# Kernel tuning notes

Hardware: AMD Instinct MI355X
Metric: run time of the kernel (lower is better)

The kernel has to match this reference:

```python
import jax, jax.numpy as jnp
import numpy as np

EPS = 1e-6
AREA_WIDTH = 3
NHEAD = 8
DIM = 16


def _skew(v):
    # v: [N,3] -> [N,3,3] cross-product matrix
    x, y, z = v[..., 0], v[..., 1], v[..., 2]
    zero = jnp.zeros_like(x)
    return jnp.stack([
        jnp.stack([zero, -z, y], -1),
        jnp.stack([z, zero, -x], -1),
        jnp.stack([-y, x, zero], -1)], -2)


def _create_meshgrid(h, w):
    # kornia create_meshgrid(..., normalized=False): last dim is (x, y), row-major flatten
    xs = jnp.arange(w, dtype=jnp.float32)
    ys = jnp.arange(h, dtype=jnp.float32)
    gx, gy = jnp.meshgrid(xs, ys, indexing='xy')  # [h,w]
    return jnp.stack([gx, gy], -1).reshape(h * w, 2)  # [S,2]


def _epipolar_lines(coord, R, t, K0, K1):
    # coord [S,2]; R [N,3,3]; t [N,3,1] -> lines [N,S,3] (unit-normalized a,b), mode [N,S]
    S = coord.shape[0]
    p = jnp.concatenate([coord, jnp.ones((S, 1), coord.dtype)], -1)  # [S,3]
    E = _skew(t[..., 0]) @ R                                         # [t]_x R
    F = jnp.swapaxes(jnp.linalg.inv(K1), -1, -2) @ E @ jnp.linalg.inv(K0)
    lines = jnp.einsum('nij,sj->nsi', F, p)
    n = jnp.linalg.norm(lines[..., :2], axis=-1, keepdims=True)
    lines = lines / jnp.maximum(n, 1e-12)
    mode = jnp.abs(lines[..., 1]) >= jnp.abs(lines[..., 0])  # True: solve y(x) (|b|>=|a|)
    return lines, mode


def _get_mask(lines, mode, coord, area_width):
    # lines [N,L,3], mode [N,L], coord [S,2] -> within [N,L,S]
    a, b, c = lines[..., 0], lines[..., 1], lines[..., 2]
    xs, ys = coord[:, 0], coord[:, 1]
    hw = area_width / 2.0
    safe = lambda d: jnp.where(jnp.abs(d) < 1e-12, 1e-12, d)
    cy = (-a / safe(b))[..., None] * xs + (-c / safe(b))[..., None]  # [N,L,S]
    cx = (-b / safe(a))[..., None] * ys + (-c / safe(a))[..., None]
    wy = (ys < cy + hw) & (ys > cy - hw)
    wx = (xs < cx + hw) & (xs > cx - hw)
    return jnp.where(mode[..., None], wy, wx)


def _gather_index(within, C):
    # sort-based top-C compaction, index 0 doubles as padding (faithful to source)
    S = within.shape[-1]
    idx = jnp.arange(S, dtype=jnp.int32)
    ti = jnp.where(within, idx[None, None, :], 0)
    ti = jnp.sort(ti, axis=-1)[..., -C:]
    return ti, ti != 0


def _feature_map(x):
    return jax.nn.elu(x) + 1.0


def reference(queries, keys, values, solved_sample, K0, K1, R, t, h0c, w0c, scale):
    N, L, H, D = queries.shape
    sol = np.asarray(solved_sample).astype(bool)  # static split of the batch
    sol_idx = np.nonzero(sol)[0]
    uns_idx = np.nonzero(~sol)[0]
    Q = _feature_map(queries)
    K = _feature_map(keys)
    out = jnp.zeros((N, L, H, D), queries.dtype)

    if sol_idx.size > 0:  # epipolar-gathered candidate attention, direction '0to1'
        coord = _create_meshgrid(h0c, w0c)
        K0s = K0[sol_idx].at[:, :2, :].mul(1.0 / scale)
        K1s = K1[sol_idx].at[:, :2, :].mul(1.0 / scale)
        C = max(h0c, w0c) * AREA_WIDTH
        lines, mode = _epipolar_lines(coord, R[sol_idx], t[sol_idx], K0s, K1s)
        within = _get_mask(lines, mode, coord, AREA_WIDTH)       # [Ns,L,S]
        index, mask = _gather_index(within, C)                    # [Ns,L,C]
        Ns = sol_idx.size
        n_ix = jnp.arange(Ns)[:, None, None]
        Qs = Q[sol_idx]
        Ks = K[sol_idx][n_ix, index]            # [Ns,L,C,H,D]
        Vs = values[sol_idx][n_ix, index]
        m = mask[..., None, None].astype(Ks.dtype)
        Ks = Ks * m
        Vs = Vs * m / C
        KV = jnp.einsum('nlchd,nlchv->nlhdv', Ks, Vs)
        Z = 1.0 / (jnp.einsum('nlhd,nlhd->nlh', Qs, Ks.sum(2)) + EPS)
        out = out.at[sol_idx].set(jnp.einsum('nlhd,nlhdv,nlh->nlhv', Qs, KV, Z) * C)

    if uns_idx.size > 0:  # plain linear attention
        Qu, Ku, Vu = Q[uns_idx], K[uns_idx], values[uns_idx]
        S = Ku.shape[1]
        KV = jnp.einsum('nshd,nshv->nhdv', Ku, Vu / S)
        Z = 1.0 / (jnp.einsum('nlhd,nhd->nlh', Qu, Ku.sum(1)) + EPS)
        out = out.at[uns_idx].set(jnp.einsum('nlhd,nhdv,nlh->nlhv', Qu, KV, Z) * S)
    return out


def setup_inputs() -> dict:
    key = jax.random.key(0)
    kq, kk, kv = jax.random.split(key, 3)
    N, H, D = 4, NHEAD, DIM
    h0c, w0c = 48, 64
    L = h0c * w0c
    queries = jax.random.normal(kq, (N, L, H, D), jnp.float32)
    keys = jax.random.normal(kk, (N, L, H, D), jnp.float32)
    values = jax.random.normal(kv, (N, L, H, D), jnp.float32)
    solved_sample = jnp.array([True, True, False, False])
    Kmat = np.array([[600., 0., 256.], [0., 600., 192.], [0., 0., 1.]], np.float32)
    K0 = jnp.asarray(np.tile(Kmat, (N, 1, 1)))
    Rl, tl = [], []
    for i in range(N):
        th = 0.05 * (i + 1)
        Rl.append(np.array([[np.cos(th), 0., np.sin(th)], [0., 1., 0.],
                            [-np.sin(th), 0., np.cos(th)]], np.float32))
        tl.append(np.array([[0.2 + 0.01 * i], [0.05], [0.02]], np.float32))
    R = jnp.asarray(np.stack(Rl))
    t = jnp.asarray(np.stack(tl))
    return {"queries": queries, "keys": keys, "values": values,
            "solved_sample": solved_sample, "K0": K0, "K1": K0, "R": R, "t": t,
            "h0c": h0c, "w0c": w0c, "scale": 8}
```

## Files before the change

### kernel.cpp

```cpp
#include <hip/hip_runtime.h>
#include <math.h>

#define NHEAD 8
#define DIM   16
#define EPSF  1e-6f
#define KVCH  8

typedef _Float16 half2_t __attribute__((ext_vector_type(2)));
typedef _Float16 half4_t __attribute__((ext_vector_type(4)));

#if defined(__has_builtin)
#if __has_builtin(__builtin_amdgcn_fdot2)
#define HAVE_FDOT2 1
#endif
#endif

__device__ __forceinline__ float dot2(half2_t a, half2_t b, float c) {
#ifdef HAVE_FDOT2
    return __builtin_amdgcn_fdot2(a, b, c, false);
#else
    return c + (float)a.x * (float)b.x + (float)a.y * (float)b.y;
#endif
}

__device__ __forceinline__ bool solved_flag(const void* p, int i) {
    const unsigned int* u = (const unsigned int*)p;
    unsigned int v0 = u[0];
    if (v0 <= 1u)             return u[i] != 0u;
    if (v0 == 0x3F800000u)    return ((const float*)p)[i] != 0.0f;
    return ((const unsigned char*)p)[i] != 0;
}

__device__ __forceinline__ float fm(float x) {
    return x > 0.f ? x + 1.f : expf(x);
}

__device__ void inv3d(const double* M, double* inv) {
    double det = M[0]*(M[4]*M[8]-M[5]*M[7]) - M[1]*(M[3]*M[8]-M[5]*M[6]) + M[2]*(M[3]*M[7]-M[4]*M[6]);
    double id = 1.0 / det;
    inv[0] =  (M[4]*M[8]-M[5]*M[7])*id;
    inv[1] = -(M[1]*M[8]-M[2]*M[7])*id;
    inv[2] =  (M[1]*M[5]-M[2]*M[4])*id;
    inv[3] = -(M[3]*M[8]-M[5]*M[6])*id;
    inv[4] =  (M[0]*M[8]-M[2]*M[6])*id;
    inv[5] = -(M[0]*M[5]-M[2]*M[3])*id;
    inv[6] =  (M[3]*M[7]-M[4]*M[6])*id;
    inv[7] = -(M[0]*M[7]-M[1]*M[6])*id;
    inv[8] =  (M[0]*M[4]-M[1]*M[3])*id;
}

__device__ void compute_F_one(const float* K0, const float* K1, const float* R,
                              const float* t, float invs, float* Fout, int n) {
    double A[9], B[9];
    for (int i = 0; i < 9; ++i) {
        float a = K0[n*9 + i], b = K1[n*9 + i];
        if (i < 6) { a *= invs; b *= invs; }
        A[i] = (double)a; B[i] = (double)b;
    }
    double iA[9], iB[9];
    inv3d(A, iA); inv3d(B, iB);
    double tx = t[n*3+0], ty = t[n*3+1], tz = t[n*3+2];
    double S[9] = {0.0,-tz,ty, tz,0.0,-tx, -ty,tx,0.0};
    double E[9], M[9];
    for (int i = 0; i < 3; ++i)
        for (int j = 0; j < 3; ++j) {
            double s = 0.0;
            for (int k = 0; k < 3; ++k) s += S[i*3+k] * (double)R[n*9 + k*3 + j];
            E[i*3+j] = s;
        }
    for (int i = 0; i < 3; ++i)
        for (int j = 0; j < 3; ++j) {
            double s = 0.0;
            for (int k = 0; k < 3; ++k) s += E[i*3+k] * iA[k*3+j];
            M[i*3+j] = s;
        }
    for (int i = 0; i < 3; ++i)
        for (int j = 0; j < 3; ++j) {
            double s = 0.0;
            for (int k = 0; k < 3; ++k) s += iB[k*3+i] * M[k*3+j];
            Fout[n*9 + i*3 + j] = (float)s;
        }
}

__launch_bounds__(256)
__global__ void prep_kv(const float4* __restrict__ Kr4, const float4* __restrict__ Vr4,
                        _Float16* __restrict__ KVh, int n4,
                        const float* __restrict__ Kr, const float* __restrict__ Vr,
                        const void* __restrict__ flags,
                        float* __restrict__ KVp, float* __restrict__ Ksp,
                        const float* __restrict__ K0, const float* __restrict__ K1,
                        const float* __restrict__ R,  const float* __restrict__ t,
                        const int* __restrict__ scale_p, float* __restrict__ Fout,
                        int N, int L, int PB) {
    if ((int)blockIdx.x < PB) {
        int i = blockIdx.x * 256 + threadIdx.x;
        if (i < n4) {
            float4 k = Kr4[i];
            float4 v = Vr4[i];
            half4_t kh = { (_Float16)fm(k.x), (_Float16)fm(k.y), (_Float16)fm(k.z), (_Float16)fm(k.w) };
            half4_t vh = { (_Float16)v.x, (_Float16)v.y, (_Float16)v.z, (_Float16)v.w };
            int r = i >> 5;
            int w = (i & 31) << 2;
            *(half4_t*)(KVh + (size_t)r * 256 + w)       = kh;
            *(half4_t*)(KVh + (size_t)r * 256 + 128 + w) = vh;
        }
        if (blockIdx.x == 0 && threadIdx.x < (unsigned)N) {
            float invs = 1.0f / (float)(*scale_p);
            compute_F_one(K0, K1, R, t, invs, Fout, threadIdx.x);
        }
    } else {
        int kb = blockIdx.x - PB;
        int chunk = kb & (KVCH - 1);
        int h = (kb >> 3) & 7;
        int n = kb >> 6;
        if (n >= N || solved_flag(flags, n)) return;
        int tdx = threadIdx.x;
        int d = tdx >> 4, v = tdx & 15;
        int rowsPer = (L + KVCH - 1) / KVCH;
        int r0 = chunk * rowsPer;
        int r1 = min(r0 + rowsPer, L);
        const float* Kb = Kr + (size_t)n * L * (NHEAD * DIM) + h * DIM;
        const float* Vb = Vr + (size_t)n * L * (NHEAD * DIM) + h * DIM;
        float acc = 0.f, ks = 0.f;
        #pragma unroll 8
        for (int s = r0; s < r1; ++s) {
            float kd = fm(Kb[(size_t)s * (NHEAD * DIM) + d]);
            float vv = Vb[(size_t)s * (NHEAD * DIM) + v];
            acc += kd * vv;
            ks  += kd;
        }
        KVp[(((size_t)chunk * N + n) * NHEAD + h) * 256 + (d << 4) + v] = acc;
        if (v == 0) Ksp[(((size_t)chunk * N + n) * NHEAD + h) * 16 + d] = ks;
    }
}

struct Buf {
    uint4 kl, kh, vl, vh;
    float msk;
};
union H16 { uint4 u; half2_t h[4]; _Float16 e[8]; };

__device__ __forceinline__ void issue(Buf& b, const char* KVb, int base16,
                                      float slope, float inter, int oo, float c1,
                                      int ob, int outerN, int innerMax, int sI, int sO) {
    int io = ob + oo;
    float fo = (float)io;
    float cc = fmaf(slope, fo, inter);
    float lo = cc - 1.5f;
    float fl = floorf(lo);
    float fi = fl + c1;
    int ii = (int)fi;
    bool val = (io < outerN) & (ii >= 0) & (ii < innerMax) & (fi > lo) & (fi < cc + 1.5f);
    int s2 = ii * sI + io * sO;
    val = val && (s2 != 0);
    int off = ((val ? s2 : 0) << 9) + base16;
    const char* p = KVb + off;
    b.kl = *(const uint4*)(p);
    b.kh = *(const uint4*)(p + 128);
    b.vl = *(const uint4*)(p + 256);
    b.vh = *(const uint4*)(p + 384);
    b.msk = val ? 1.f : 0.f;
}

__device__ __forceinline__ void consume(const Buf& b, const half2_t* ql, const half2_t* qh,
                                        float* aL, float* aH, float& dL, float& dH) {
    H16 k0, k1, v0, v1;
    k0.u = b.kl; k1.u = b.kh; v0.u = b.vl; v1.u = b.vh;
    float sA = 0.f, sB = 0.f;
    #pragma unroll
    for (int i = 0; i < 4; ++i) {
        sA = dot2(ql[i], k0.h[i], sA);
        sB = dot2(qh[i], k1.h[i], sB);
    }
    sA += __shfl_xor(sA, 1);
    sB += __shfl_xor(sB, 1);
    float scL = sA * b.msk;
    float scH = sB * b.msk;
    dL += scL; dH += scH;
    #pragma unroll
    for (int i = 0; i < 8; ++i) {
        aL[i] = fmaf(scL, (float)v0.e[i], aL[i]);
        aH[i] = fmaf(scH, (float)v1.e[i], aH[i]);
    }
}

__launch_bounds__(256)
__global__ void mega(const float* __restrict__ Qr,
                     const _Float16* __restrict__ KVh,
                     const void* __restrict__ flags,  const float* __restrict__ F,
                     const float* __restrict__ KVp,   const float* __restrict__ Ksp,
                     float* __restrict__ outp,
                     const int* __restrict__ h0c_p, const int* __restrict__ w0c_p,
                     int N, int L, int Bs) {
    if ((int)blockIdx.x < Bs) {
        int wid = (blockIdx.x << 2) | (threadIdx.x >> 6);
        wid = __builtin_amdgcn_readfirstlane(wid);
        int lane = threadIdx.x & 63;
        int n = wid / L;
        if (n >= N) return;
        if (!solved_flag(flags, n)) return;
        int s = wid - n * L;
        int W  = *w0c_p;
        int Hc = *h0c_p;
        float px = (float)(s % W);
        float py = (float)(s / W);

        const float* Fn = F + n * 9;
        float a = Fn[0]*px + Fn[1]*py + Fn[2];
        float b = Fn[3]*px + Fn[4]*py + Fn[5];
        float c = Fn[6]*px + Fn[7]*py + Fn[8];
        float nrm = sqrtf(a*a + b*b);
        float mdiv = fmaxf(nrm, 1e-12f);
        a /= mdiv; b /= mdiv; c /= mdiv;
        bool mode = fabsf(b) >= fabsf(a);

        float slope, inter;
        int outerN, innerMax, sI, sO;
        if (mode) {
            float bs = (fabsf(b) < 1e-12f) ? 1e-12f : b;
            slope = -a / bs; inter = -c / bs;
            outerN = W; innerMax = Hc; sI = W; sO = 1;
        } else {
            float as = (fabsf(a) < 1e-12f) ? 1e-12f : a;
            slope = -b / as; inter = -c / as;
            outerN = Hc; innerMax = W; sI = 1; sO = W;
        }

        int cL  = lane >> 3;
        int sub = lane & 7;
        int hL  = sub >> 1;
        int dh  = sub & 1;
        int base16 = sub << 4;

        const float* qbase = Qr + (size_t)wid * (NHEAD * DIM);
        half2_t ql[4], qh[4];
        {
            const float4* qa = (const float4*)(qbase + hL * DIM + dh * 8);
            float4 a0 = qa[0], a1 = qa[1];
            ql[0] = (half2_t){ (_Float16)fm(a0.x), (_Float16)fm(a0.y) };
            ql[1] = (half2_t){ (_Float16)fm(a0.z), (_Float16)fm(a0.w) };
            ql[2] = (half2_t){ (_Float16)fm(a1.x), (_Float16)fm(a1.y) };
            ql[3] = (half2_t){ (_Float16)fm(a1.z), (_Float16)fm(a1.w) };
            const float4* qb = (const float4*)(qbase + (hL + 4) * DIM + dh * 8);
            float4 b0 = qb[0], b1 = qb[1];
            qh[0] = (half2_t){ (_Float16)fm(b0.x), (_Float16)fm(b0.y) };
            qh[1] = (half2_t){ (_Float16)fm(b0.z), (_Float16)fm(b0.w) };
            qh[2] = (half2_t){ (_Float16)fm(b1.x), (_Float16)fm(b1.y) };
            qh[3] = (half2_t){ (_Float16)fm(b1.z), (_Float16)fm(b1.w) };
        }

        const char* KVb = (const char*)KVh + (size_t)n * L * 512;

        int mm0 = cL, mm1 = 8 + cL, mm2 = 16 + cL;
        int oo0 = mm0 / 3, oo1 = mm1 / 3, oo2 = mm2 / 3;
        float c10 = (float)(1 + (mm0 - 3 * oo0));
        float c11 = (float)(1 + (mm1 - 3 * oo1));
        float c12 = (float)(1 + (mm2 - 3 * oo2));

        int totalC = outerN * 3;
        int NM3 = (totalC + 23) / 24;

        float accL[8], accH[8];
        #pragma unroll
        for (int i = 0; i < 8; ++i) { accL[i] = 0.f; accH[i] = 0.f; }
        float denL = 0.f, denH = 0.f;

        Buf A, B, C;
        issue(A, KVb, base16, slope, inter, oo0, c10, 0, outerN, innerMax, sI, sO);
        issue(B, KVb, base16, slope, inter, oo1, c11, 0, outerN, innerMax, sI, sO);
        int ob = 0;
        for (int k = 0; k < NM3; ++k) {
            issue(C, KVb, base16, slope, inter, oo2, c12, ob, outerN, innerMax, sI, sO);
            consume(A, ql, qh, accL, accH, denL, denH);
            int obn = ob + 8;
            issue(A, KVb, base16, slope, inter, oo0, c10, obn, outerN, innerMax, sI, sO);
            consume(B, ql, qh, accL, accH, denL, denH);
            issue(B, KVb, base16, slope, inter, oo1, c11, obn, outerN, innerMax, sI, sO);
            consume(C, ql, qh, accL, accH, denL, denH);
            ob = obn;
        }

        #pragma unroll
        for (int j = 0; j < 8; ++j) {
            accL[j] += __shfl_xor(accL[j], 8);
            accL[j] += __shfl_xor(accL[j], 16);
            accL[j] += __shfl_xor(accL[j], 32);
            accH[j] += __shfl_xor(accH[j], 8);
            accH[j] += __shfl_xor(accH[j], 16);
            accH[j] += __shfl_xor(accH[j], 32);
        }
        denL += __shfl_xor(denL, 8);
        denL += __shfl_xor(denL, 16);
        denL += __shfl_xor(denL, 32);
        denH += __shfl_xor(denH, 8);
        denH += __shfl_xor(denH, 16);
        denH += __shfl_xor(denH, 32);

        if (lane < 8) {
            float rL = 1.0f / (denL + EPSF);
            float rH = 1.0f / (denH + EPSF);
            float* op = outp + (size_t)wid * (NHEAD * DIM) + lane * 8;
            float4 o0 = { accL[0]*rL, accL[1]*rL, accL[2]*rL, accL[3]*rL };
            float4 o1 = { accL[4]*rL, accL[5]*rL, accL[6]*rL, accL[7]*rL };
            ((float4*)op)[0] = o0;
            ((float4*)op)[1] = o1;
            float4 o2 = { accH[0]*rH, accH[1]*rH, accH[2]*rH, accH[3]*rH };
            float4 o3 = { accH[4]*rH, accH[5]*rH, accH[6]*rH, accH[7]*rH };
            ((float4*)(op + 64))[0] = o2;
            ((float4*)(op + 64))[1] = o3;
        }
    } else {
        long long tot2 = (long long)N * L * NHEAD * DIM / 2;
        long long idx2 = (long long)(blockIdx.x - Bs) * 256 + threadIdx.x;
        if (idx2 >= tot2) return;
        int p = (int)(idx2 & 63);
        int h = p >> 3;
        int v = (p & 7) * 2;
        long long ns = idx2 >> 6;
        int n = (int)(ns / L);
        if (solved_flag(flags, n)) return;
        const float* qrow = Qr + ns * (NHEAD * DIM) + h * DIM;
        float num0 = 0.f, num1 = 0.f, den = 0.f;
        #pragma unroll
        for (int d = 0; d < 16; ++d) {
            float qd = fm(qrow[d]);
            #pragma unroll
            for (int cch = 0; cch < KVCH; ++cch) {
                const float2 kv2 = *(const float2*)(KVp + (((size_t)cch * N + n) * NHEAD + h) * 256 + (d << 4) + v);
                num0 += qd * kv2.x;
                num1 += qd * kv2.y;
                den  += qd * Ksp[(((size_t)cch * N + n) * NHEAD + h) * 16 + d] * (1.0f / 16.0f);
            }
        }
        den *= 16.0f;
        float rdiv = 1.0f / (den + EPSF);
        size_t ob = ns * (NHEAD * DIM) + h * DIM + v;
        outp[ob]     = num0 * rdiv;
        outp[ob + 1] = num1 * rdiv;
    }
}

extern "C" void kernel_launch(void* const* d_in, const int* in_sizes, int n_in,
                              void* d_out, int out_size, void* d_ws, size_t ws_size,
                              hipStream_t stream) {
    const float* Qr   = (const float*)d_in[0];
    const float* Kr   = (const float*)d_in[1];
    const float* Vr   = (const float*)d_in[2];
    const void*  flag = d_in[3];
    const float* K0   = (const float*)d_in[4];
    const float* K1   = (const float*)d_in[5];
    const float* R    = (const float*)d_in[6];
    const float* t    = (const float*)d_in[7];
    const int*   h0c  = (const int*)d_in[8];
    const int*   w0c  = (const int*)d_in[9];
    const int*   scl  = (const int*)d_in[10];

    int N = in_sizes[3];
    int T = in_sizes[0];
    int L = T / (N * NHEAD * DIM);

    _Float16* KVh = (_Float16*)d_ws;
    float* Fm   = (float*)(KVh + (size_t)2 * T);
    float* KVp  = Fm + (size_t)N * 9;
    float* Ksp  = KVp + (size_t)KVCH * N * NHEAD * 256;

    float* outp = (float*)d_out;

    int n4 = T / 4;
    int PB = (n4 + 255) / 256;
    int KB = N * NHEAD * KVCH;
    prep_kv<<<PB + KB, 256, 0, stream>>>((const float4*)Kr, (const float4*)Vr,
                                         KVh, n4, Kr, Vr, flag, KVp, Ksp,
                                         K0, K1, R, t, scl, Fm, N, L, PB);

    int Bs = (N * L + 3) / 4;
    long long tot2 = (long long)N * L * NHEAD * DIM / 2;
    int Bu = (int)((tot2 + 255) / 256);
    mega<<<Bs + Bu, 256, 0, stream>>>(Qr, KVh, flag, Fm, KVp, Ksp, outp,
                                      h0c, w0c, N, L, Bs);
}
```

Before: 173.4 us.

## Split each query's epipolar sweep across two waves with LDS reduction

Each query is now processed by two wavefronts instead of one. Each wave takes alternating 24-column chunks of the epipolar band, and the partial accumulators and denominators are combined through shared memory behind a block barrier. The aim is more parallelism and a shorter serial dependency chain per query. In exchange, the cross-iteration software prefetch is dropped (all three buffers are now issued and consumed within one iteration), and a __syncthreads is added that relies on both queries in a block taking the same early-return path.

```diff
diff --git a/kernel.cpp b/kernel.cpp
--- a/kernel.cpp
+++ b/kernel.cpp
@@ -192,14 +192,18 @@
                      float* __restrict__ outp,
                      const int* __restrict__ h0c_p, const int* __restrict__ w0c_p,
                      int N, int L, int Bs) {
+    __shared__ float red[2][8][18];
     if ((int)blockIdx.x < Bs) {
-        int wid = (blockIdx.x << 2) | (threadIdx.x >> 6);
-        wid = __builtin_amdgcn_readfirstlane(wid);
-        int lane = threadIdx.x & 63;
-        int n = wid / L;
+        int tid   = threadIdx.x;
+        int qslot = tid >> 7;
+        int wh    = (tid >> 6) & 1;
+        int lane  = tid & 63;
+        int qidx  = (blockIdx.x << 1) | qslot;
+        qidx = __builtin_amdgcn_readfirstlane(qidx);
+        int n = qidx / L;
         if (n >= N) return;
         if (!solved_flag(flags, n)) return;
-        int s = wid - n * L;
+        int s = qidx - n * L;
         int W  = *w0c_p;
         int Hc = *h0c_p;
         float px = (float)(s % W);
@@ -232,7 +236,7 @@
         int dh  = sub & 1;
         int base16 = sub << 4;
 
-        const float* qbase = Qr + (size_t)wid * (NHEAD * DIM);
+        const float* qbase = Qr + (size_t)qidx * (NHEAD * DIM);
         half2_t ql[4], qh[4];
         {
             const float4* qa = (const float4*)(qbase + hL * DIM + dh * 8);
@@ -265,19 +269,15 @@
         for (int i = 0; i < 8; ++i) { accL[i] = 0.f; accH[i] = 0.f; }
         float denL = 0.f, denH = 0.f;
 
-        Buf A, B, C;
-        issue(A, KVb, base16, slope, inter, oo0, c10, 0, outerN, innerMax, sI, sO);
-        issue(B, KVb, base16, slope, inter, oo1, c11, 0, outerN, innerMax, sI, sO);
-        int ob = 0;
-        for (int k = 0; k < NM3; ++k) {
+        for (int k = wh; k < NM3; k += 2) {
+            int ob = k << 3;
+            Buf A, B, C;
+            issue(A, KVb, base16, slope, inter, oo0, c10, ob, outerN, innerMax, sI, sO);
+            issue(B, KVb, base16, slope, inter, oo1, c11, ob, outerN, innerMax, sI, sO);
             issue(C, KVb, base16, slope, inter, oo2, c12, ob, outerN, innerMax, sI, sO);
             consume(A, ql, qh, accL, accH, denL, denH);
-            int obn = ob + 8;
-            issue(A, KVb, base16, slope, inter, oo0, c10, obn, outerN, innerMax, sI, sO);
             consume(B, ql, qh, accL, accH, denL, denH);
-            issue(B, KVb, base16, slope, inter, oo1, c11, obn, outerN, innerMax, sI, sO);
             consume(C, ql, qh, accL, accH, denL, denH);
-            ob = obn;
         }
 
         #pragma unroll
@@ -296,10 +296,28 @@
         denH += __shfl_xor(denH, 16);
         denH += __shfl_xor(denH, 32);
 
-        if (lane < 8) {
+        if (wh == 1 && lane < 8) {
+            #pragma unroll
+            for (int i = 0; i < 8; ++i) {
+                red[qslot][lane][i]     = accL[i];
+                red[qslot][lane][8 + i] = accH[i];
+            }
+            red[qslot][lane][16] = denL;
+            red[qslot][lane][17] = denH;
+        }
+        __syncthreads();
+        if (wh == 0 && lane < 8) {
+            #pragma unroll
+            for (int i = 0; i < 8; ++i) {
+                accL[i] += red[qslot][lane][i];
+                accH[i] += red[qslot][lane][8 + i];
+            }
+            denL += red[qslot][lane][16];
+            denH += red[qslot][lane][17];
+
             float rL = 1.0f / (denL + EPSF);
             float rH = 1.0f / (denH + EPSF);
-            float* op = outp + (size_t)wid * (NHEAD * DIM) + lane * 8;
+            float* op = outp + (size_t)qidx * (NHEAD * DIM) + lane * 8;
             float4 o0 = { accL[0]*rL, accL[1]*rL, accL[2]*rL, accL[3]*rL };
             float4 o1 = { accL[4]*rL, accL[5]*rL, accL[6]*rL, accL[7]*rL };
             ((float4*)op)[0] = o0;
@@ -373,7 +391,7 @@
                                          KVh, n4, Kr, Vr, flag, KVp, Ksp,
                                          K0, K1, R, t, scl, Fm, N, L, PB);
 
-    int Bs = (N * L + 3) / 4;
+    int Bs = (N * L + 1) / 2;
     long long tot2 = (long long)N * L * NHEAD * DIM / 2;
     int Bu = (int)((tot2 + 255) / 256);
     mega<<<Bs + Bu, 256, 0, stream>>>(Qr, KVh, flag, Fm, KVp, Ksp, outp,
```

After: 185.3 us. +6.9%, slower.

## Compact solved samples into XCD-interleaved block groups and drop software pipelining

Applied to the files above, without the earlier changes.

Each block now works out which samples are solved and maps its index modulo 8 onto a group assigned to one solved sample. This packs the work for solved samples into the launched blocks, so no blocks exit early for unsolved samples, and keeps each sample's K/V working set on a subset of the chiplets. The rotating triple-buffer prefetch is replaced by issuing and consuming all three buffers inside each iteration. That simplifies register use but loses the overlap of loads with compute across iterations. Every block also scans the flags, which adds a little overhead.

```diff
diff --git a/kernel.cpp b/kernel.cpp
--- a/kernel.cpp
+++ b/kernel.cpp
@@ -193,17 +193,31 @@
                      const int* __restrict__ h0c_p, const int* __restrict__ w0c_p,
                      int N, int L, int Bs) {
     if ((int)blockIdx.x < Bs) {
-        int wid = (blockIdx.x << 2) | (threadIdx.x >> 6);
-        wid = __builtin_amdgcn_readfirstlane(wid);
+        int g  = blockIdx.x & 7;
+        int gb = blockIdx.x >> 3;
+
+        int scnt = 0, smap[8];
+        for (int i = 0; i < N && i < 8; ++i)
+            if (solved_flag(flags, i)) smap[scnt++] = i;
+        if (scnt == 0) return;
+
+        int r   = (g * scnt) >> 3;
+        int g0  = (r * 8 + scnt - 1) / scnt;
+        int ng  = ((r + 1) * 8 + scnt - 1) / scnt - g0;
+        int sub = g - g0;
+        int n   = smap[r];
+
+        int wv  = threadIdx.x >> 6;
         int lane = threadIdx.x & 63;
-        int n = wid / L;
-        if (n >= N) return;
-        if (!solved_flag(flags, n)) return;
-        int s = wid - n * L;
+        int q = (gb * ng + sub) * 4 + wv;
+        if (q >= L) return;
+        q = __builtin_amdgcn_readfirstlane(q);
+        int qidx = n * L + q;
+
         int W  = *w0c_p;
         int Hc = *h0c_p;
-        float px = (float)(s % W);
-        float py = (float)(s / W);
+        float px = (float)(q % W);
+        float py = (float)(q / W);
 
         const float* Fn = F + n * 9;
         float a = Fn[0]*px + Fn[1]*py + Fn[2];
@@ -226,13 +240,13 @@
             outerN = Hc; innerMax = W; sI = 1; sO = W;
         }
 
-        int cL  = lane >> 3;
-        int sub = lane & 7;
-        int hL  = sub >> 1;
-        int dh  = sub & 1;
-        int base16 = sub << 4;
-
-        const float* qbase = Qr + (size_t)wid * (NHEAD * DIM);
+        int cL   = lane >> 3;
+        int sub8 = lane & 7;
+        int hL   = sub8 >> 1;
+        int dh   = sub8 & 1;
+        int base16 = sub8 << 4;
+
+        const float* qbase = Qr + (size_t)qidx * (NHEAD * DIM);
         half2_t ql[4], qh[4];
         {
             const float4* qa = (const float4*)(qbase + hL * DIM + dh * 8);
@@ -265,19 +279,15 @@
         for (int i = 0; i < 8; ++i) { accL[i] = 0.f; accH[i] = 0.f; }
         float denL = 0.f, denH = 0.f;
 
-        Buf A, B, C;
-        issue(A, KVb, base16, slope, inter, oo0, c10, 0, outerN, innerMax, sI, sO);
-        issue(B, KVb, base16, slope, inter, oo1, c11, 0, outerN, innerMax, sI, sO);
-        int ob = 0;
         for (int k = 0; k < NM3; ++k) {
+            int ob = k << 3;
+            Buf A, B, C;
+            issue(A, KVb, base16, slope, inter, oo0, c10, ob, outerN, innerMax, sI, sO);
+            issue(B, KVb, base16, slope, inter, oo1, c11, ob, outerN, innerMax, sI, sO);
             issue(C, KVb, base16, slope, inter, oo2, c12, ob, outerN, innerMax, sI, sO);
             consume(A, ql, qh, accL, accH, denL, denH);
-            int obn = ob + 8;
-            issue(A, KVb, base16, slope, inter, oo0, c10, obn, outerN, innerMax, sI, sO);
             consume(B, ql, qh, accL, accH, denL, denH);
-            issue(B, KVb, base16, slope, inter, oo1, c11, obn, outerN, innerMax, sI, sO);
             consume(C, ql, qh, accL, accH, denL, denH);
-            ob = obn;
         }
 
         #pragma unroll
@@ -299,7 +309,7 @@
         if (lane < 8) {
             float rL = 1.0f / (denL + EPSF);
             float rH = 1.0f / (denH + EPSF);
-            float* op = outp + (size_t)wid * (NHEAD * DIM) + lane * 8;
+            float* op = outp + (size_t)qidx * (NHEAD * DIM) + lane * 8;
             float4 o0 = { accL[0]*rL, accL[1]*rL, accL[2]*rL, accL[3]*rL };
             float4 o1 = { accL[4]*rL, accL[5]*rL, accL[6]*rL, accL[7]*rL };
             ((float4*)op)[0] = o0;
@@ -373,7 +383,8 @@
                                          KVh, n4, Kr, Vr, flag, KVp, Ksp,
                                          K0, K1, R, t, scl, Fm, N, L, PB);
 
-    int Bs = (N * L + 3) / 4;
+    int GB = (L + 7) / 8;
+    int Bs = 8 * GB;
     long long tot2 = (long long)N * L * NHEAD * DIM / 2;
     int Bu = (int)((tot2 + 255) / 256);
     mega<<<Bs + Bu, 256, 0, stream>>>(Qr, KVh, flag, Fm, KVp, Ksp, outp,
```

Result: slower. 179.6 us (+3.6%).
